# Kernel tuning notes

Hardware: AMD Instinct MI355X
Metric: run time of the kernel (lower is better)

## Reference

```python
import jax, jax.numpy as jnp
import numpy as np

B, NUM_ROIS, NUM_GT = 32, 8192, 128
NUM_SAMPLED = 512
POS_FRAC = 0.25
BACKGROUND = 0.0
VARIANCE = np.array([0.1, 0.1, 0.2, 0.2], np.float32)  # [dy, dx, dh, dw]
IMG = 1024.0


def _make_boxes(key, shape):
    # valid yxyx boxes: positive height/width, inside image
    kc, ks = jax.random.split(key)
    c = jax.random.uniform(kc, shape[:-1] + (2,), minval=0.2, maxval=0.8) * IMG
    hw = jax.random.uniform(ks, shape[:-1] + (2,), minval=0.05, maxval=0.3) * IMG
    return jnp.concatenate([c - 0.5 * hw, c + 0.5 * hw], axis=-1)


def setup_inputs() -> dict:
    key = jax.random.key(0)
    k1, k2, k3, k4 = jax.random.split(key, 4)
    rois = _make_boxes(k1, (B, NUM_ROIS, 4))
    gt_boxes = _make_boxes(k2, (B, NUM_GT, 4))
    gt_classes = jax.random.randint(k3, (B, NUM_GT, 1), 1, 81).astype(jnp.float32)
    # uniform noise used by balanced_sample (channel 0 for positives, 1 for negatives)
    sample_noise = jax.random.uniform(k4, (B, NUM_ROIS + NUM_GT, 2), dtype=jnp.float32)
    return {"rois": rois, "gt_boxes": gt_boxes, "gt_classes": gt_classes,
            "sample_noise": sample_noise}


def _compute_iou(a, b):
    # a: [B,N,4], b: [B,G,4] in yxyx; use_masking=True -> padded (-1) boxes get iou=-1
    a_ = a[:, :, None, :]   # [B,N,1,4]
    b_ = b[:, None, :, :]   # [B,1,G,4]
    iy = jnp.maximum(jnp.minimum(a_[..., 2], b_[..., 2]) - jnp.maximum(a_[..., 0], b_[..., 0]), 0.0)
    ix = jnp.maximum(jnp.minimum(a_[..., 3], b_[..., 3]) - jnp.maximum(a_[..., 1], b_[..., 1]), 0.0)
    inter = iy * ix
    area_a = (a[..., 2] - a[..., 0]) * (a[..., 3] - a[..., 1])  # [B,N]
    area_b = (b[..., 2] - b[..., 0]) * (b[..., 3] - b[..., 1])  # [B,G]
    union = area_a[:, :, None] + area_b[:, None, :] - inter
    iou = inter / jnp.maximum(union, 1e-8)
    mask_a = jnp.all(a == -1.0, axis=-1)  # [B,N] padded rois
    mask_b = jnp.all(b == -1.0, axis=-1)  # [B,G] padded gt
    masked = mask_a[:, :, None] | mask_b[:, None, :]
    return jnp.where(masked, -1.0, iou)


def _encode_deltas(anchors, boxes):
    # yxyx -> (dy,dx,dh,dw)/variance
    ah = anchors[..., 2] - anchors[..., 0]
    aw = anchors[..., 3] - anchors[..., 1]
    acy = anchors[..., 0] + 0.5 * ah
    acx = anchors[..., 1] + 0.5 * aw
    bh = boxes[..., 2] - boxes[..., 0]
    bw = boxes[..., 3] - boxes[..., 1]
    bcy = boxes[..., 0] + 0.5 * bh
    bcx = boxes[..., 1] + 0.5 * bw
    d = jnp.stack([(bcy - acy) / ah, (bcx - acx) / aw,
                   jnp.log(bh / ah), jnp.log(bw / aw)], axis=-1)
    return d / jnp.asarray(VARIANCE, d.dtype)


def _balanced_sample(pos, neg, noise, num_samples, pos_frac):
    # returns float indicator [B,N]: 1.0 for sampled rois
    num_pos = int(num_samples * pos_frac)
    num_neg = num_samples - num_pos
    b, n = pos.shape
    pos_scores = jnp.where(pos, noise[..., 0], -1.0)
    neg_scores = jnp.where(neg, noise[..., 1], -1.0)
    _, pi = jax.lax.top_k(pos_scores, num_pos)
    _, ni = jax.lax.top_k(neg_scores, num_neg)
    rows = jnp.arange(b)[:, None]
    # only mark picks that are actually positive/negative (handles scarcity)
    pv = jnp.take_along_axis(pos, pi, axis=-1).astype(jnp.float32)
    nv = jnp.take_along_axis(neg, ni, axis=-1).astype(jnp.float32)
    ind = jnp.zeros((b, n), jnp.float32)
    ind = ind.at[rows, pi].add(pv)
    ind = ind.at[rows, ni].add(nv)  # pos/neg disjoint -> stays in {0,1}
    return ind


def _gather(t, idx):
    # t: [B,M,D], idx: [B,K] -> [B,K,D]
    return jnp.take_along_axis(t, idx[..., None], axis=1)


def reference(rois, gt_boxes, gt_classes, sample_noise):
    # append_gt_boxes=True
    rois_all = jnp.concatenate([rois, gt_boxes], axis=1)  # [B, N+G, 4]
    sim = _compute_iou(rois_all, gt_boxes)                # [B, N+G, G]
    matched_cols = jnp.argmax(sim, axis=-1)               # [B, N+G]
    max_iou = jnp.max(sim, axis=-1)
    # ArgmaxBoxMatcher(thresholds=[0.0,0.5], match_values=[-2,-1,1])
    matched_vals = jnp.where(max_iou >= 0.5, 1, jnp.where(max_iou >= 0.0, -1, -2))
    positive = matched_vals == 1
    negative = matched_vals == -1
    background = ~positive                                # [B, N+G]

    matched_gt_classes = _gather(gt_classes, matched_cols)
    matched_gt_classes = jnp.where(background[..., None], BACKGROUND, matched_gt_classes)
    matched_gt_boxes = _gather(gt_boxes, matched_cols)
    encoded = _encode_deltas(rois_all, matched_gt_boxes)
    encoded = jnp.where(background[..., None], 0.0, encoded)

    indicators = _balanced_sample(positive, negative, sample_noise, NUM_SAMPLED, POS_FRAC)
    sampled_indicators, sampled_idx = jax.lax.top_k(indicators, NUM_SAMPLED)

    sampled_rois = _gather(rois_all, sampled_idx)
    sampled_gt_boxes = _gather(encoded, sampled_idx)
    sampled_gt_classes = _gather(matched_gt_classes, sampled_idx)
    sampled_box_weights = _gather(positive[..., None].astype(gt_boxes.dtype), sampled_idx)
    sampled_class_weights = sampled_indicators[..., None].astype(gt_classes.dtype)
    return (sampled_rois, sampled_gt_boxes, sampled_box_weights,
            sampled_gt_classes, sampled_class_weights)
```

## Files before the change

kernel.cpp:

```cpp
#include <hip/hip_runtime.h>
#include <cstdint>

#define NB 32
#define NROIS 8192
#define NGT 128
#define NALL (NROIS + NGT)
#define NSAMP 512
#define KPOS 128
#define KNEG 384
#define BCAP 1024
#define TS 1024
#define CH 9

__global__ __launch_bounds__(256) void k_match(
    const float* __restrict__ rois,
    const float* __restrict__ gt,
    const float* __restrict__ noise,
    int* __restrict__ mword)
{
  __shared__ float4 sg[NGT];
  __shared__ float sab[NGT];
  __shared__ int s_any;
  __shared__ float mbi[128], mbu[128];
  __shared__ int mbc[128];

  const int b = blockIdx.y;
  const int tid = threadIdx.x;
  const int r = tid & 127;
  const int half = tid >> 7;
  const float4* gt4 = reinterpret_cast<const float4*>(gt) + (size_t)b * NGT;
  const float4* rois4 = reinterpret_cast<const float4*>(rois) + (size_t)b * NROIS;

  if (tid == 0) s_any = 0;
  bool mflag = false;
  if (tid < NGT) {
    float4 g0 = gt4[tid];
    sg[tid] = g0;
    sab[tid] = (g0.z - g0.x) * (g0.w - g0.y);
    mflag = (g0.x == -1.0f) && (g0.y == -1.0f) && (g0.z == -1.0f) && (g0.w == -1.0f);
  }

  const int i = blockIdx.x * 128 + r;
  float4 A = (blockIdx.x < 64) ? rois4[i] : gt4[r];
  const float aar = (A.z - A.x) * (A.w - A.y);
  const bool ma = (A.x == -1.0f) && (A.y == -1.0f) && (A.z == -1.0f) && (A.w == -1.0f);

  __syncthreads();
  if (mflag || ma) atomicOr(&s_any, 1);
  __syncthreads();

  if (s_any == 0) {
    const int jb = half * 64;
    float bi[4], bu[4];
    int bc[4];
    #pragma unroll
    for (int c = 0; c < 4; ++c) { bi[c] = 0.0f; bu[c] = 1.0f; bc[c] = jb + c * 16; }

    #pragma unroll 4
    for (int jj = 0; jj < 16; ++jj) {
      #pragma unroll
      for (int c = 0; c < 4; ++c) {
        const int j = jb + c * 16 + jj;
        const float4 g = sg[j];
        const float ab = (g.z - g.x) * (g.w - g.y);
        float iy = fmaxf(fminf(A.z, g.z) - fmaxf(A.x, g.x), 0.0f);
        float ix = fmaxf(fminf(A.w, g.w) - fmaxf(A.y, g.y), 0.0f);
        float inter = iy * ix;
        float uc = fmaxf((aar + ab) - inter, 1e-8f);
        const bool win = (inter * bu[c]) > (bi[c] * uc);
        bi[c] = win ? inter : bi[c];
        bu[c] = win ? uc : bu[c];
        bc[c] = win ? j : bc[c];
      }
    }
    float qi = bi[0], qu = bu[0];
    int qc = bc[0];
    #pragma unroll
    for (int c = 1; c < 4; ++c) {
      const bool win = (bi[c] * qu) > (qi * bu[c]);
      qi = win ? bi[c] : qi; qu = win ? bu[c] : qu; qc = win ? bc[c] : qc;
    }
    if (half) { mbi[r] = qi; mbu[r] = qu; mbc[r] = qc; }
    __syncthreads();
    if (!half) {
      const float oi = mbi[r], ou = mbu[r];
      const int oc = mbc[r];
      const bool win = (oi * qu) > (qi * ou);
      qi = win ? oi : qi; qu = win ? ou : qu; qc = win ? oc : qc;

      int code;
      {
        #pragma clang fp contract(off)
        const float4 g = sg[qc];
        float iy = fmaxf(fminf(A.z, g.z) - fmaxf(A.x, g.x), 0.0f);
        float ix = fmaxf(fminf(A.w, g.w) - fmaxf(A.y, g.y), 0.0f);
        float inter = iy * ix;
        float ab = (g.z - g.x) * (g.w - g.y);
        float uni = (aar + ab) - inter;
        float bb = inter / fmaxf(uni, 1e-8f);
        code = (bb >= 0.5f) ? 3 : ((bb >= 0.0f) ? 1 : 0);
      }
      float2 nz = reinterpret_cast<const float2*>(noise)[(size_t)b * NALL + i];
      float v = (code == 3) ? nz.x : nz.y;
      int bin = (int)(v * 1024.0f);
      bin = bin < 0 ? 0 : (bin > 1023 ? 1023 : bin);
      mword[(size_t)b * NALL + i] = qc | (code << 7) | (bin << 9);
    }
  } else {
    if (!half) {
      #pragma clang fp contract(off)
      float bb = -3.0e38f;
      int cc = 0;
      for (int j = 0; j < NGT; ++j) {
        float4 gg = sg[j];
        const bool mj = (gg.x == -1.0f) && (gg.y == -1.0f) && (gg.z == -1.0f) && (gg.w == -1.0f);
        float iy = fmaxf(fminf(A.z, gg.z) - fmaxf(A.x, gg.x), 0.0f);
        float ix = fmaxf(fminf(A.w, gg.w) - fmaxf(A.y, gg.y), 0.0f);
        float inter = iy * ix;
        float uni = (aar + sab[j]) - inter;
        float iou = inter / fmaxf(uni, 1e-8f);
        if (ma || mj) iou = -1.0f;
        if (iou > bb) { bb = iou; cc = j; }
      }
      int code = (bb >= 0.5f) ? 3 : ((bb >= 0.0f) ? 1 : 0);
      float2 nz = reinterpret_cast<const float2*>(noise)[(size_t)b * NALL + i];
      float v = (code == 3) ? nz.x : nz.y;
      int bin = (int)(v * 1024.0f);
      bin = bin < 0 ? 0 : (bin > 1023 ? 1023 : bin);
      mword[(size_t)b * NALL + i] = cc | (code << 7) | (bin << 9);
    }
  }
}

__device__ __forceinline__ int block_incl_scan(int v, int tid, int* wsum) {
  __syncthreads();
  int s = v;
  #pragma unroll
  for (int off = 1; off < 64; off <<= 1) {
    int u = __shfl_up(s, off);
    if ((tid & 63) >= off) s += u;
  }
  const int wid = tid >> 6;
  if ((tid & 63) == 63) wsum[wid] = s;
  __syncthreads();
  if (wid == 0) {
    const int lane = tid & 63;
    int w = (lane < (TS >> 6)) ? wsum[lane] : 0;
    #pragma unroll
    for (int off = 1; off < (TS >> 6); off <<= 1) {
      int u = __shfl_up(w, off);
      if (lane >= off) w += u;
    }
    if (lane < (TS >> 6)) wsum[lane] = w;
  }
  __syncthreads();
  return s + (wid ? wsum[wid - 1] : 0);
}

__global__ __launch_bounds__(TS) void k_select(
    const int* __restrict__ mword,
    const float* __restrict__ noise,
    const float* __restrict__ rois,
    const float* __restrict__ gt,
    const float* __restrict__ gtcls,
    float* __restrict__ out)
{
  #pragma clang fp contract(off)
  const int b = blockIdx.x;
  const int tid = threadIdx.x;

  __shared__ int hist[1024];
  __shared__ int wsum[TS >> 6];
  __shared__ int s_total;
  __shared__ float bval[2][BCAP];
  __shared__ int bidx_[2][BCAP];
  __shared__ int bcnt[2];
  __shared__ int s_bstar[2], s_need[2];
  __shared__ unsigned char ind[NALL];
  __shared__ unsigned short sorder[NSAMP];

  int ew[CH];

  hist[tid] = 0;
  if (tid < 2) bcnt[tid] = 0;

  #pragma unroll
  for (int k = 0; k < CH; ++k) {
    const int i = tid + k * TS;
    int w = 0;
    if (i < NALL) {
      ind[i] = 0;
      w = mword[(size_t)b * NALL + i];
    }
    ew[k] = w;
  }
  __syncthreads();
  #pragma unroll
  for (int k = 0; k < CH; ++k) {
    const int w = ew[k];
    if (w & 0x80) atomicAdd(&hist[w >> 9], (w & 0x100) ? 1 : (1 << 16));
  }
  __syncthreads();

  const int c = hist[tid];
  const int incl = block_incl_scan(c, tid, wsum);
  if (tid == TS - 1) s_total = incl;
  __syncthreads();
  const int total = s_total;

  #pragma unroll
  for (int p = 0; p < 2; ++p) {
    const int want = p ? KNEG : KPOS;
    const int sh = p ? 16 : 0;
    const int tot = (total >> sh) & 0xFFFF;
    if (tot >= want) {
      const int inc = (incl >> sh) & 0xFFFF;
      const int cp = (c >> sh) & 0xFFFF;
      const int above = tot - inc;
      if (above < want && above + cp >= want) {
        s_bstar[p] = tid; s_need[p] = want - above;
      }
    }
  }
  __syncthreads();

  const bool selall0 = ((total & 0xFFFF) < KPOS);
  const bool selall1 = (((total >> 16) & 0xFFFF) < KNEG);

  #pragma unroll
  for (int k = 0; k < CH; ++k) {
    const int w = ew[k];
    if (w & 0x80) {
      const int i = tid + k * TS;
      const int p = (w & 0x100) ? 0 : 1;
      const bool selall = p ? selall1 : selall0;
      const int bin = w >> 9;
      if (selall || bin > s_bstar[p]) {
        ind[i] = 1;
      } else if (bin == s_bstar[p]) {
        int pos = atomicAdd(&bcnt[p], 1);
        if (pos < BCAP) {
          bval[p][pos] = noise[((size_t)b * NALL + i) * 2 + p];
          bidx_[p][pos] = i;
        }
      }
    }
  }
  __syncthreads();

  #pragma unroll
  for (int p = 0; p < 2; ++p) {
    const bool selall = p ? selall1 : selall0;
    if (selall) continue;
    int cnt = bcnt[p]; if (cnt > BCAP) cnt = BCAP;
    const int need = s_need[p];
    for (int x = tid; x < cnt; x += TS) {
      const float v = bval[p][x];
      const int id = bidx_[p][x];
      int rank = 0;
      for (int y = 0; y < cnt; ++y) {
        const float vy = bval[p][y];
        const int iy2 = bidx_[p][y];
        rank += (vy > v) || (vy == v && iy2 < id);
      }
      if (rank < need) ind[id] = 1;
    }
  }
  __syncthreads();

  const int start = tid * CH;
  const int end = (start + CH < NALL) ? (start + CH) : NALL;
  int cnt1 = 0;
  for (int i = start; i < end; ++i) cnt1 += ind[i];
  const int incl1 = block_incl_scan(cnt1, tid, wsum);
  if (tid == TS - 1) s_total = incl1;
  __syncthreads();
  const int K1 = s_total;
  int ones_before = incl1 - cnt1;
  const int nzero = NSAMP - K1;
  for (int i = start; i < end; ++i) {
    if (ind[i]) {
      sorder[ones_before] = (unsigned short)i;
      ones_before++;
    } else {
      const int zrank = i - ones_before;
      if (zrank < nzero) sorder[K1 + zrank] = (unsigned short)i;
    }
  }
  __syncthreads();

  if (tid < NSAMP) {
    const int s = tid;
    const int idx = sorder[s];
    const size_t t = (size_t)b * NSAMP + s;

    float4 A = (idx < NROIS)
      ? reinterpret_cast<const float4*>(rois)[(size_t)b * NROIS + idx]
      : reinterpret_cast<const float4*>(gt)[(size_t)b * NGT + (idx - NROIS)];

    const int w = mword[(size_t)b * NALL + idx];
    const int col = w & 0x7F;
    const bool pos = (((w >> 7) & 3) == 3);

    float e0 = 0.f, e1 = 0.f, e2 = 0.f, e3 = 0.f, cls = 0.f;
    if (pos) {
      float4 G = reinterpret_cast<const float4*>(gt)[(size_t)b * NGT + col];
      float ah = A.z - A.x, aw = A.w - A.y;
      float acy = A.x + 0.5f * ah, acx = A.y + 0.5f * aw;
      float bh = G.z - G.x, bw = G.w - G.y;
      float bcy = G.x + 0.5f * bh, bcx = G.y + 0.5f * bw;
      e0 = ((bcy - acy) / ah) / 0.1f;
      e1 = ((bcx - acx) / aw) / 0.1f;
      e2 = logf(bh / ah) / 0.2f;
      e3 = logf(bw / aw) / 0.2f;
      cls = gtcls[(size_t)b * NGT + col];
    }

    float* o_rois = out;
    float* o_enc  = out + (size_t)NB * NSAMP * 4;
    float* o_bw   = out + (size_t)NB * NSAMP * 8;
    float* o_cls  = o_bw + (size_t)NB * NSAMP;
    float* o_cw   = o_cls + (size_t)NB * NSAMP;

    reinterpret_cast<float4*>(o_rois)[t] = A;
    float4 E; E.x = e0; E.y = e1; E.z = e2; E.w = e3;
    reinterpret_cast<float4*>(o_enc)[t] = E;
    o_bw[t]  = pos ? 1.0f : 0.0f;
    o_cls[t] = cls;
    o_cw[t]  = (s < K1) ? 1.0f : 0.0f;
  }
}

extern "C" void kernel_launch(void* const* d_in, const int* in_sizes, int n_in,
                              void* d_out, int out_size, void* d_ws, size_t ws_size,
                              hipStream_t stream) {
  const float* rois  = (const float*)d_in[0];
  const float* gt    = (const float*)d_in[1];
  const float* gtcls = (const float*)d_in[2];
  const float* noise = (const float*)d_in[3];
  float* out = (float*)d_out;

  int* mword = (int*)d_ws;

  dim3 g1(NALL / 128, NB);
  k_match<<<g1, 256, 0, stream>>>(rois, gt, noise, mword);
  k_select<<<NB, TS, 0, stream>>>(mword, noise, rois, gt, gtcls, out);
}
```

Baseline: 39.27 us.

## Prune IoU candidates with a coarse spatial grid of GT overlap bitmasks

Adds a pre-pass kernel that builds, per batch, a 16x16 grid of 64-pixel cells with a 128-bit mask of the GT boxes overlapping each cell. The match kernel then ORs the masks of the cells an ROI covers and evaluates IoU only for those candidate GTs, instead of scanning all 128. It also moves from two threads per ROI to one. This reduces the arithmetic but introduces data-dependent, divergent loops and an extra launch; with large boxes the candidate sets may remain big.

```diff
diff --git a/kernel.cpp b/kernel.cpp
--- a/kernel.cpp
+++ b/kernel.cpp
@@ -12,22 +12,47 @@
 #define TS 1024
 #define CH 9
 
+__global__ __launch_bounds__(256) void k_cells(
+    const float* __restrict__ gt,
+    uint4* __restrict__ cmask)
+{
+  __shared__ float4 sg[NGT];
+  const int b = blockIdx.x;
+  const int t = threadIdx.x;
+  if (t < NGT) sg[t] = reinterpret_cast<const float4*>(gt)[b * NGT + t];
+  __syncthreads();
+
+  const int cy = t >> 4, cx = t & 15;
+  const float y0 = (cy == 0)  ? -3.0e38f : cy * 64.0f;
+  const float y1 = (cy == 15) ?  3.0e38f : (cy + 1) * 64.0f;
+  const float x0 = (cx == 0)  ? -3.0e38f : cx * 64.0f;
+  const float x1 = (cx == 15) ?  3.0e38f : (cx + 1) * 64.0f;
+
+  unsigned mm[4] = {0u, 0u, 0u, 0u};
+  #pragma unroll
+  for (int j = 0; j < NGT; ++j) {
+    const float4 g = sg[j];
+    const bool ov = (g.x <= y1) && (g.z >= y0) && (g.y <= x1) && (g.w >= x0);
+    mm[j >> 5] |= ((unsigned)ov) << (j & 31);
+  }
+  uint4 o; o.x = mm[0]; o.y = mm[1]; o.z = mm[2]; o.w = mm[3];
+  cmask[(size_t)b * 256 + t] = o;
+}
+
 __global__ __launch_bounds__(256) void k_match(
     const float* __restrict__ rois,
     const float* __restrict__ gt,
     const float* __restrict__ noise,
+    const uint4* __restrict__ cmask,
     int* __restrict__ mword)
 {
   __shared__ float4 sg[NGT];
   __shared__ float sab[NGT];
+  __shared__ uint4 scm[256];
   __shared__ int s_any;
-  __shared__ float mbi[128], mbu[128];
-  __shared__ int mbc[128];
 
   const int b = blockIdx.y;
   const int tid = threadIdx.x;
-  const int r = tid & 127;
-  const int half = tid >> 7;
   const float4* gt4 = reinterpret_cast<const float4*>(gt) + (size_t)b * NGT;
   const float4* rois4 = reinterpret_cast<const float4*>(rois) + (size_t)b * NROIS;
 
@@ -39,97 +64,94 @@
     sab[tid] = (g0.z - g0.x) * (g0.w - g0.y);
     mflag = (g0.x == -1.0f) && (g0.y == -1.0f) && (g0.z == -1.0f) && (g0.w == -1.0f);
   }
-
-  const int i = blockIdx.x * 128 + r;
-  float4 A = (blockIdx.x < 64) ? rois4[i] : gt4[r];
+  scm[tid] = cmask[(size_t)b * 256 + tid];
+
+  const int i = blockIdx.x * 256 + tid;
+  const bool act = (i < NALL);
+  float4 A = act ? ((i < NROIS) ? rois4[i] : gt4[i - NROIS]) : rois4[0];
   const float aar = (A.z - A.x) * (A.w - A.y);
-  const bool ma = (A.x == -1.0f) && (A.y == -1.0f) && (A.z == -1.0f) && (A.w == -1.0f);
+  const bool ma = act && (A.x == -1.0f) && (A.y == -1.0f) && (A.z == -1.0f) && (A.w == -1.0f);
 
   __syncthreads();
   if (mflag || ma) atomicOr(&s_any, 1);
   __syncthreads();
 
+  if (!act) return;
+
+  int cc;
+  int code;
+
   if (s_any == 0) {
-    const int jb = half * 64;
-    float bi[4], bu[4];
-    int bc[4];
-    #pragma unroll
-    for (int c = 0; c < 4; ++c) { bi[c] = 0.0f; bu[c] = 1.0f; bc[c] = jb + c * 16; }
-
-    #pragma unroll 4
-    for (int jj = 0; jj < 16; ++jj) {
-      #pragma unroll
-      for (int c = 0; c < 4; ++c) {
-        const int j = jb + c * 16 + jj;
-        const float4 g = sg[j];
-        const float ab = (g.z - g.x) * (g.w - g.y);
-        float iy = fmaxf(fminf(A.z, g.z) - fmaxf(A.x, g.x), 0.0f);
-        float ix = fmaxf(fminf(A.w, g.w) - fmaxf(A.y, g.y), 0.0f);
-        float inter = iy * ix;
-        float uc = fmaxf((aar + ab) - inter, 1e-8f);
-        const bool win = (inter * bu[c]) > (bi[c] * uc);
-        bi[c] = win ? inter : bi[c];
-        bu[c] = win ? uc : bu[c];
-        bc[c] = win ? j : bc[c];
+    const float inv = 1.0f / 64.0f;
+    int cy0 = (int)(A.x * inv), cy1 = (int)(A.z * inv);
+    int cx0 = (int)(A.y * inv), cx1 = (int)(A.w * inv);
+    cy0 = cy0 < 0 ? 0 : (cy0 > 15 ? 15 : cy0);
+    cy1 = cy1 < 0 ? 0 : (cy1 > 15 ? 15 : cy1);
+    cx0 = cx0 < 0 ? 0 : (cx0 > 15 ? 15 : cx0);
+    cx1 = cx1 < 0 ? 0 : (cx1 > 15 ? 15 : cx1);
+
+    unsigned mm0 = 0u, mm1 = 0u, mm2 = 0u, mm3 = 0u;
+    for (int cy = cy0; cy <= cy1; ++cy) {
+      for (int cx = cx0; cx <= cx1; ++cx) {
+        const uint4 cm = scm[(cy << 4) + cx];
+        mm0 |= cm.x; mm1 |= cm.y; mm2 |= cm.z; mm3 |= cm.w;
       }
     }
-    float qi = bi[0], qu = bu[0];
-    int qc = bc[0];
-    #pragma unroll
-    for (int c = 1; c < 4; ++c) {
-      const bool win = (bi[c] * qu) > (qi * bu[c]);
-      qi = win ? bi[c] : qi; qu = win ? bu[c] : qu; qc = win ? bc[c] : qc;
-    }
-    if (half) { mbi[r] = qi; mbu[r] = qu; mbc[r] = qc; }
-    __syncthreads();
-    if (!half) {
-      const float oi = mbi[r], ou = mbu[r];
-      const int oc = mbc[r];
-      const bool win = (oi * qu) > (qi * ou);
-      qi = win ? oi : qi; qu = win ? ou : qu; qc = win ? oc : qc;
-
-      int code;
-      {
-        #pragma clang fp contract(off)
-        const float4 g = sg[qc];
-        float iy = fmaxf(fminf(A.z, g.z) - fmaxf(A.x, g.x), 0.0f);
-        float ix = fmaxf(fminf(A.w, g.w) - fmaxf(A.y, g.y), 0.0f);
-        float inter = iy * ix;
-        float ab = (g.z - g.x) * (g.w - g.y);
-        float uni = (aar + ab) - inter;
-        float bb = inter / fmaxf(uni, 1e-8f);
-        code = (bb >= 0.5f) ? 3 : ((bb >= 0.0f) ? 1 : 0);
-      }
-      float2 nz = reinterpret_cast<const float2*>(noise)[(size_t)b * NALL + i];
-      float v = (code == 3) ? nz.x : nz.y;
-      int bin = (int)(v * 1024.0f);
-      bin = bin < 0 ? 0 : (bin > 1023 ? 1023 : bin);
-      mword[(size_t)b * NALL + i] = qc | (code << 7) | (bin << 9);
+
+    float bi = 0.0f, bu = 1.0f;
+    int bc = 0;
+    auto eval = [&](int j) {
+      const float4 g = sg[j];
+      const float ab = (g.z - g.x) * (g.w - g.y);
+      float iy = fmaxf(fminf(A.z, g.z) - fmaxf(A.x, g.x), 0.0f);
+      float ix = fmaxf(fminf(A.w, g.w) - fmaxf(A.y, g.y), 0.0f);
+      float inter = iy * ix;
+      float uc = fmaxf((aar + ab) - inter, 1e-8f);
+      const bool win = (inter * bu) > (bi * uc);
+      bi = win ? inter : bi;
+      bu = win ? uc : bu;
+      bc = win ? j : bc;
+    };
+    { unsigned m = mm0; while (m) { const int j =      __builtin_ctz(m); m &= m - 1; eval(j); } }
+    { unsigned m = mm1; while (m) { const int j = 32 + __builtin_ctz(m); m &= m - 1; eval(j); } }
+    { unsigned m = mm2; while (m) { const int j = 64 + __builtin_ctz(m); m &= m - 1; eval(j); } }
+    { unsigned m = mm3; while (m) { const int j = 96 + __builtin_ctz(m); m &= m - 1; eval(j); } }
+    cc = bc;
+
+    {
+      #pragma clang fp contract(off)
+      const float4 g = sg[cc];
+      float iy = fmaxf(fminf(A.z, g.z) - fmaxf(A.x, g.x), 0.0f);
+      float ix = fmaxf(fminf(A.w, g.w) - fmaxf(A.y, g.y), 0.0f);
+      float inter = iy * ix;
+      float ab = (g.z - g.x) * (g.w - g.y);
+      float uni = (aar + ab) - inter;
+      float bb = inter / fmaxf(uni, 1e-8f);
+      code = (bb >= 0.5f) ? 3 : ((bb >= 0.0f) ? 1 : 0);
     }
   } else {
-    if (!half) {
-      #pragma clang fp contract(off)
-      float bb = -3.0e38f;
-      int cc = 0;
-      for (int j = 0; j < NGT; ++j) {
-        float4 gg = sg[j];
-        const bool mj = (gg.x == -1.0f) && (gg.y == -1.0f) && (gg.z == -1.0f) && (gg.w == -1.0f);
-        float iy = fmaxf(fminf(A.z, gg.z) - fmaxf(A.x, gg.x), 0.0f);
-        float ix = fmaxf(fminf(A.w, gg.w) - fmaxf(A.y, gg.y), 0.0f);
-        float inter = iy * ix;
-        float uni = (aar + sab[j]) - inter;
-        float iou = inter / fmaxf(uni, 1e-8f);
-        if (ma || mj) iou = -1.0f;
-        if (iou > bb) { bb = iou; cc = j; }
-      }
-      int code = (bb >= 0.5f) ? 3 : ((bb >= 0.0f) ? 1 : 0);
-      float2 nz = reinterpret_cast<const float2*>(noise)[(size_t)b * NALL + i];
-      float v = (code == 3) ? nz.x : nz.y;
-      int bin = (int)(v * 1024.0f);
-      bin = bin < 0 ? 0 : (bin > 1023 ? 1023 : bin);
-      mword[(size_t)b * NALL + i] = cc | (code << 7) | (bin << 9);
-    }
-  }
+    #pragma clang fp contract(off)
+    float bb = -3.0e38f;
+    cc = 0;
+    for (int j = 0; j < NGT; ++j) {
+      float4 gg = sg[j];
+      const bool mj = (gg.x == -1.0f) && (gg.y == -1.0f) && (gg.z == -1.0f) && (gg.w == -1.0f);
+      float iy = fmaxf(fminf(A.z, gg.z) - fmaxf(A.x, gg.x), 0.0f);
+      float ix = fmaxf(fminf(A.w, gg.w) - fmaxf(A.y, gg.y), 0.0f);
+      float inter = iy * ix;
+      float uni = (aar + sab[j]) - inter;
+      float iou = inter / fmaxf(uni, 1e-8f);
+      if (ma || mj) iou = -1.0f;
+      if (iou > bb) { bb = iou; cc = j; }
+    }
+    code = (bb >= 0.5f) ? 3 : ((bb >= 0.0f) ? 1 : 0);
+  }
+
+  float2 nz = reinterpret_cast<const float2*>(noise)[(size_t)b * NALL + i];
+  float v = (code == 3) ? nz.x : nz.y;
+  int bin = (int)(v * 1024.0f);
+  bin = bin < 0 ? 0 : (bin > 1023 ? 1023 : bin);
+  mword[(size_t)b * NALL + i] = cc | (code << 7) | (bin << 9);
 }
 
 __device__ __forceinline__ int block_incl_scan(int v, int tid, int* wsum) {
@@ -340,9 +362,12 @@
   const float* noise = (const float*)d_in[3];
   float* out = (float*)d_out;
 
-  int* mword = (int*)d_ws;
-
-  dim3 g1(NALL / 128, NB);
-  k_match<<<g1, 256, 0, stream>>>(rois, gt, noise, mword);
+  uint8_t* ws = (uint8_t*)d_ws;
+  int* mword = (int*)ws;
+  uint4* cmask = (uint4*)(ws + (size_t)NB * NALL * sizeof(int));
+
+  k_cells<<<NB, 256, 0, stream>>>(gt, cmask);
+  dim3 g1((NALL + 255) / 256, NB);
+  k_match<<<g1, 256, 0, stream>>>(rois, gt, noise, cmask, mword);
   k_select<<<NB, TS, 0, stream>>>(mword, noise, rois, gt, gtcls, out);
 }
```

Measured after the change: 56.07 us. +42.8%, slower.

## Register-block four ROIs per thread and split GT boxes across wavefronts in k_match

Applied to the files above, without the earlier changes.

Each block now covers 256 ROIs instead of 128. Every thread holds 4 ROI boxes in registers and scans a 32-GT slice chosen by its wavefront, so each shared-memory GT load and area computation is reused across 4 ROIs. Partial argmax results go through shared memory and are reduced across the 4 wavefronts, and each thread then finalises one ROI. This cuts shared-memory traffic per IoU and halves the block count, at the cost of more registers and a bounds check on the last partial block.

```diff
diff --git a/kernel.cpp b/kernel.cpp
--- a/kernel.cpp
+++ b/kernel.cpp
@@ -21,13 +21,14 @@
   __shared__ float4 sg[NGT];
   __shared__ float sab[NGT];
   __shared__ int s_any;
-  __shared__ float mbi[128], mbu[128];
-  __shared__ int mbc[128];
+  __shared__ float pbi[4][64][4];
+  __shared__ float pbu[4][64][4];
+  __shared__ int   pbc[4][64][4];
 
   const int b = blockIdx.y;
   const int tid = threadIdx.x;
-  const int r = tid & 127;
-  const int half = tid >> 7;
+  const int lane = tid & 63;
+  const int q = tid >> 6;
   const float4* gt4 = reinterpret_cast<const float4*>(gt) + (size_t)b * NGT;
   const float4* rois4 = reinterpret_cast<const float4*>(rois) + (size_t)b * NROIS;
 
@@ -39,95 +40,111 @@
     sab[tid] = (g0.z - g0.x) * (g0.w - g0.y);
     mflag = (g0.x == -1.0f) && (g0.y == -1.0f) && (g0.z == -1.0f) && (g0.w == -1.0f);
   }
-
-  const int i = blockIdx.x * 128 + r;
-  float4 A = (blockIdx.x < 64) ? rois4[i] : gt4[r];
-  const float aar = (A.z - A.x) * (A.w - A.y);
-  const bool ma = (A.x == -1.0f) && (A.y == -1.0f) && (A.z == -1.0f) && (A.w == -1.0f);
-
-  __syncthreads();
-  if (mflag || ma) atomicOr(&s_any, 1);
+  __syncthreads();
+
+  const int base = blockIdx.x * 256;
+  float4 A[4];
+  float aar[4];
+  bool act[4];
+  bool maAny = false;
+  #pragma unroll
+  for (int r = 0; r < 4; ++r) {
+    const int idx = base + lane + 64 * r;
+    act[r] = (idx < NALL);
+    A[r] = act[r] ? ((idx < NROIS) ? rois4[idx] : sg[idx - NROIS]) : rois4[0];
+    aar[r] = (A[r].z - A[r].x) * (A[r].w - A[r].y);
+    maAny |= act[r] && (A[r].x == -1.0f) && (A[r].y == -1.0f) && (A[r].z == -1.0f) && (A[r].w == -1.0f);
+  }
+  if (mflag || maAny) atomicOr(&s_any, 1);
   __syncthreads();
 
   if (s_any == 0) {
-    const int jb = half * 64;
-    float bi[4], bu[4];
+    float bi[4] = {0.f, 0.f, 0.f, 0.f};
+    float bu[4] = {1.f, 1.f, 1.f, 1.f};
     int bc[4];
     #pragma unroll
-    for (int c = 0; c < 4; ++c) { bi[c] = 0.0f; bu[c] = 1.0f; bc[c] = jb + c * 16; }
-
-    #pragma unroll 4
-    for (int jj = 0; jj < 16; ++jj) {
+    for (int r = 0; r < 4; ++r) bc[r] = 32 * q;
+
+    const float4* p = &sg[32 * q];
+    #pragma unroll 8
+    for (int jj = 0; jj < 32; ++jj) {
+      const float4 g = p[jj];
+      const float ab = (g.z - g.x) * (g.w - g.y);
       #pragma unroll
-      for (int c = 0; c < 4; ++c) {
-        const int j = jb + c * 16 + jj;
-        const float4 g = sg[j];
-        const float ab = (g.z - g.x) * (g.w - g.y);
-        float iy = fmaxf(fminf(A.z, g.z) - fmaxf(A.x, g.x), 0.0f);
-        float ix = fmaxf(fminf(A.w, g.w) - fmaxf(A.y, g.y), 0.0f);
+      for (int r = 0; r < 4; ++r) {
+        float iy = fmaxf(fminf(A[r].z, g.z) - fmaxf(A[r].x, g.x), 0.0f);
+        float ix = fmaxf(fminf(A[r].w, g.w) - fmaxf(A[r].y, g.y), 0.0f);
         float inter = iy * ix;
-        float uc = fmaxf((aar + ab) - inter, 1e-8f);
-        const bool win = (inter * bu[c]) > (bi[c] * uc);
-        bi[c] = win ? inter : bi[c];
-        bu[c] = win ? uc : bu[c];
-        bc[c] = win ? j : bc[c];
-      }
-    }
-    float qi = bi[0], qu = bu[0];
-    int qc = bc[0];
+        float uc = fmaxf((aar[r] + ab) - inter, 1e-8f);
+        const bool win = (inter * bu[r]) > (bi[r] * uc);
+        bi[r] = win ? inter : bi[r];
+        bu[r] = win ? uc : bu[r];
+        bc[r] = win ? (32 * q + jj) : bc[r];
+      }
+    }
     #pragma unroll
-    for (int c = 1; c < 4; ++c) {
-      const bool win = (bi[c] * qu) > (qi * bu[c]);
-      qi = win ? bi[c] : qi; qu = win ? bu[c] : qu; qc = win ? bc[c] : qc;
-    }
-    if (half) { mbi[r] = qi; mbu[r] = qu; mbc[r] = qc; }
+    for (int r = 0; r < 4; ++r) {
+      pbi[q][lane][r] = bi[r];
+      pbu[q][lane][r] = bu[r];
+      pbc[q][lane][r] = bc[r];
+    }
     __syncthreads();
-    if (!half) {
-      const float oi = mbi[r], ou = mbu[r];
-      const int oc = mbc[r];
-      const bool win = (oi * qu) > (qi * ou);
-      qi = win ? oi : qi; qu = win ? ou : qu; qc = win ? oc : qc;
-
+
+    const int idx = base + lane + 64 * q;
+    if (idx < NALL) {
+      float qi = pbi[0][lane][q], qu = pbu[0][lane][q];
+      int qc = pbc[0][lane][q];
+      #pragma unroll
+      for (int qq = 1; qq < 4; ++qq) {
+        const float oi = pbi[qq][lane][q], ou = pbu[qq][lane][q];
+        const int oc = pbc[qq][lane][q];
+        const bool win = (oi * qu) > (qi * ou);
+        qi = win ? oi : qi; qu = win ? ou : qu; qc = win ? oc : qc;
+      }
       int code;
       {
         #pragma clang fp contract(off)
         const float4 g = sg[qc];
-        float iy = fmaxf(fminf(A.z, g.z) - fmaxf(A.x, g.x), 0.0f);
-        float ix = fmaxf(fminf(A.w, g.w) - fmaxf(A.y, g.y), 0.0f);
+        float iy = fmaxf(fminf(A[q].z, g.z) - fmaxf(A[q].x, g.x), 0.0f);
+        float ix = fmaxf(fminf(A[q].w, g.w) - fmaxf(A[q].y, g.y), 0.0f);
         float inter = iy * ix;
         float ab = (g.z - g.x) * (g.w - g.y);
-        float uni = (aar + ab) - inter;
+        float uni = (aar[q] + ab) - inter;
         float bb = inter / fmaxf(uni, 1e-8f);
         code = (bb >= 0.5f) ? 3 : ((bb >= 0.0f) ? 1 : 0);
       }
-      float2 nz = reinterpret_cast<const float2*>(noise)[(size_t)b * NALL + i];
+      float2 nz = reinterpret_cast<const float2*>(noise)[(size_t)b * NALL + idx];
       float v = (code == 3) ? nz.x : nz.y;
       int bin = (int)(v * 1024.0f);
       bin = bin < 0 ? 0 : (bin > 1023 ? 1023 : bin);
-      mword[(size_t)b * NALL + i] = qc | (code << 7) | (bin << 9);
+      mword[(size_t)b * NALL + idx] = qc | (code << 7) | (bin << 9);
     }
   } else {
-    if (!half) {
+    const int idx = base + lane + 64 * q;
+    if (idx < NALL) {
       #pragma clang fp contract(off)
+      const float4 Aq = A[q];
+      const float aq = aar[q];
+      const bool ma = (Aq.x == -1.0f) && (Aq.y == -1.0f) && (Aq.z == -1.0f) && (Aq.w == -1.0f);
       float bb = -3.0e38f;
       int cc = 0;
       for (int j = 0; j < NGT; ++j) {
         float4 gg = sg[j];
         const bool mj = (gg.x == -1.0f) && (gg.y == -1.0f) && (gg.z == -1.0f) && (gg.w == -1.0f);
-        float iy = fmaxf(fminf(A.z, gg.z) - fmaxf(A.x, gg.x), 0.0f);
-        float ix = fmaxf(fminf(A.w, gg.w) - fmaxf(A.y, gg.y), 0.0f);
+        float iy = fmaxf(fminf(Aq.z, gg.z) - fmaxf(Aq.x, gg.x), 0.0f);
+        float ix = fmaxf(fminf(Aq.w, gg.w) - fmaxf(Aq.y, gg.y), 0.0f);
         float inter = iy * ix;
-        float uni = (aar + sab[j]) - inter;
+        float uni = (aq + sab[j]) - inter;
         float iou = inter / fmaxf(uni, 1e-8f);
         if (ma || mj) iou = -1.0f;
         if (iou > bb) { bb = iou; cc = j; }
       }
       int code = (bb >= 0.5f) ? 3 : ((bb >= 0.0f) ? 1 : 0);
-      float2 nz = reinterpret_cast<const float2*>(noise)[(size_t)b * NALL + i];
+      float2 nz = reinterpret_cast<const float2*>(noise)[(size_t)b * NALL + idx];
       float v = (code == 3) ? nz.x : nz.y;
       int bin = (int)(v * 1024.0f);
       bin = bin < 0 ? 0 : (bin > 1023 ? 1023 : bin);
-      mword[(size_t)b * NALL + i] = cc | (code << 7) | (bin << 9);
+      mword[(size_t)b * NALL + idx] = cc | (code << 7) | (bin << 9);
     }
   }
 }
@@ -342,7 +359,7 @@
 
   int* mword = (int*)d_ws;
 
-  dim3 g1(NALL / 128, NB);
+  dim3 g1((NALL + 255) / 256, NB);
   k_match<<<g1, 256, 0, stream>>>(rois, gt, noise, mword);
   k_select<<<NB, TS, 0, stream>>>(mword, noise, rois, gt, gtcls, out);
 }
```

Result: slower. 43.15 us (+9.9%).
